# Kernel optimization log

Measured on AMD Instinct MI355X. Metric: run time of the kernel, lower is better.

Reference implementation:

```python
import jax, jax.numpy as jnp
import numpy as np

MEL = 80      # mel_dim
RED = 2       # reduction factor
D   = 256     # decoder_dim (== enc_output feature dim for dot attention)
E   = 128     # encoder_dim == prenet output dim
PRE = 256     # prenet hidden
B, T, L = 128, 500, 256


def _gru_cell(x, h, w_ih, w_hh, b_ih, b_hh):
    # PyTorch GRUCell math
    gi = x @ w_ih.T + b_ih
    gh = h @ w_hh.T + b_hh
    i_r, i_z, i_n = jnp.split(gi, 3, axis=-1)
    h_r, h_z, h_n = jnp.split(gh, 3, axis=-1)
    r = jax.nn.sigmoid(i_r + h_r)
    z = jax.nn.sigmoid(i_z + h_z)
    n = jnp.tanh(i_n + r * h_n)
    return (1.0 - z) * n + z * h


def setup_inputs() -> dict:
    key = jax.random.key(0)
    ks = jax.random.split(key, 16)
    def p(k, shape, s=0.05):
        return jax.random.normal(k, shape, dtype=jnp.float32) * s
    z = lambda n: jnp.zeros((n,), jnp.float32)
    return {
        'dec_input':  jax.random.normal(ks[0], (B, T, MEL), jnp.float32),
        'enc_output': jax.random.normal(ks[1], (B, L, D), jnp.float32),
        # prenet: mel -> 256 -> 128 (ReLU; dropout omitted for determinism)
        'pre_w1': p(ks[2], (PRE, MEL)), 'pre_b1': z(PRE),
        'pre_w2': p(ks[3], (E, PRE)),   'pre_b2': z(E),
        # attention GRUCell(encoder_dim -> decoder_dim)
        'attn_wih': p(ks[4], (3 * D, E)), 'attn_whh': p(ks[5], (3 * D, D)),
        'attn_bih': z(3 * D), 'attn_bhh': z(3 * D),
        # proj1: 2*decoder_dim -> decoder_dim
        'proj1_w': p(ks[6], (D, 2 * D)), 'proj1_b': z(D),
        # decoder GRUCells
        'rnn1_wih': p(ks[7], (3 * D, D)), 'rnn1_whh': p(ks[8], (3 * D, D)),
        'rnn1_bih': z(3 * D), 'rnn1_bhh': z(3 * D),
        'rnn2_wih': p(ks[9], (3 * D, D)), 'rnn2_whh': p(ks[10], (3 * D, D)),
        'rnn2_bih': z(3 * D), 'rnn2_bhh': z(3 * D),
        # proj2: decoder_dim -> mel_dim * reduction
        'proj2_w': p(ks[11], (MEL * RED, D)), 'proj2_b': z(MEL * RED),
    }


def reference(dec_input, enc_output,
              pre_w1, pre_b1, pre_w2, pre_b2,
              attn_wih, attn_whh, attn_bih, attn_bhh,
              proj1_w, proj1_b,
              rnn1_wih, rnn1_whh, rnn1_bih, rnn1_bhh,
              rnn2_wih, rnn2_whh, rnn2_bih, rnn2_bhh,
              proj2_w, proj2_b):
    b, t, _ = dec_input.shape

    def step(carry, frame):
        h_attn, h1, h2 = carry
        # prenet
        x = jax.nn.relu(frame @ pre_w1.T + pre_b1)
        x = jax.nn.relu(x @ pre_w2.T + pre_b2)
        # attention RNN
        h_attn = _gru_cell(x, h_attn, attn_wih, attn_whh, attn_bih, attn_bhh)
        # Luong dot attention: query = h_attn [b, D]
        scores = jnp.einsum('bd,bld->bl', h_attn, enc_output)   # [b, L]
        align = jax.nn.softmax(scores, axis=-1)
        ctx = jnp.einsum('bl,bld->bd', align, enc_output)        # [b, D]
        dec_in = jnp.concatenate([ctx, h_attn], axis=-1) @ proj1_w.T + proj1_b
        # residual GRU stack
        h1 = _gru_cell(dec_in, h1, rnn1_wih, rnn1_whh, rnn1_bih, rnn1_bhh)
        y1 = dec_in + h1
        h2 = _gru_cell(y1, h2, rnn2_wih, rnn2_whh, rnn2_bih, rnn2_bhh)
        y2 = y1 + h2
        out = y2 @ proj2_w.T + proj2_b                            # [b, MEL*RED]
        return (h_attn, h1, h2), (out, align)

    init = tuple(jnp.zeros((b, D), dec_input.dtype) for _ in range(3))
    _, (outs, aligns) = jax.lax.scan(step, init, jnp.swapaxes(dec_input, 0, 1))
    mel_out = jnp.swapaxes(outs, 0, 1).reshape(b, t * RED, MEL)  # [b, T*RED, MEL]
    alignment = jnp.transpose(aligns, (1, 2, 0))                 # [b, L, T]
    return mel_out, alignment
```

## Files before the change

### kernel.cpp

```cpp
#include <hip/hip_runtime.h>
#include <cmath>

#define B_   128
#define T_   500
#define MEL_ 80
#define RED_ 2
#define D_   256
#define E_   128
#define PRE_ 256
#define L_   256
#define TPB  1024
#define ENC_STRIDE 264
#define PTT  10

__device__ __forceinline__ float sigmoidf_(float x) { return 1.f / (1.f + expf(-x)); }
__device__ __forceinline__ float bflo(unsigned u) { return __uint_as_float(u << 16); }
__device__ __forceinline__ float bfhi(unsigned u) { return __uint_as_float(u & 0xFFFF0000u); }
__device__ __forceinline__ float bfval(ushort v) { return __uint_as_float(((unsigned)v) << 16); }
__device__ __forceinline__ ushort f2bf(float f) {
    unsigned u = __float_as_uint(f);
    return (ushort)((u + 0x7FFFu + ((u >> 16) & 1u)) >> 16);
}

__device__ __forceinline__ float acc8(uint4 u, const float* vv, float s) {
    s = fmaf(bflo(u.x), vv[0], s);
    s = fmaf(bfhi(u.x), vv[1], s);
    s = fmaf(bflo(u.y), vv[2], s);
    s = fmaf(bfhi(u.y), vv[3], s);
    s = fmaf(bflo(u.z), vv[4], s);
    s = fmaf(bfhi(u.z), vv[5], s);
    s = fmaf(bflo(u.w), vv[6], s);
    s = fmaf(bfhi(u.w), vv[7], s);
    return s;
}

template<int CH>
__device__ __forceinline__ float dotpk(const ushort* __restrict__ wp, int t, const float* v) {
    const uint4* w = reinterpret_cast<const uint4*>(wp) + (t >> 6) * (CH * 64) + (t & 63);
    float s0 = 0.f, s1 = 0.f, s2 = 0.f, s3 = 0.f;
#pragma unroll 2
    for (int c = 0; c < (CH & ~3); c += 4) {
        uint4 u0 = w[(c + 0) * 64];
        uint4 u1 = w[(c + 1) * 64];
        uint4 u2 = w[(c + 2) * 64];
        uint4 u3 = w[(c + 3) * 64];
        s0 = acc8(u0, v + (c + 0) * 8, s0);
        s1 = acc8(u1, v + (c + 1) * 8, s1);
        s2 = acc8(u2, v + (c + 2) * 8, s2);
        s3 = acc8(u3, v + (c + 3) * 8, s3);
    }
    if (CH & 2) {
        constexpr int c0 = CH & ~3;
        uint4 u0 = w[(c0 + 0) * 64];
        uint4 u1 = w[(c0 + 1) * 64];
        s0 = acc8(u0, v + (c0 + 0) * 8, s0);
        s1 = acc8(u1, v + (c0 + 1) * 8, s1);
    }
    return (s0 + s1) + (s2 + s3);
}

__device__ __forceinline__ float dotbf(const ushort* __restrict__ wrow,
                                       const float* v, int k8) {
    const uint4* w = reinterpret_cast<const uint4*>(wrow);
    float s = 0.f;
#pragma unroll 8
    for (int k = 0; k < k8; ++k) {
        uint4 u = w[k];
        const float* vv = v + k * 8;
        s = fmaf(bflo(u.x), vv[0], s);
        s = fmaf(bfhi(u.x), vv[1], s);
        s = fmaf(bflo(u.y), vv[2], s);
        s = fmaf(bfhi(u.y), vv[3], s);
        s = fmaf(bflo(u.z), vv[4], s);
        s = fmaf(bfhi(u.z), vv[5], s);
        s = fmaf(bflo(u.w), vv[6], s);
        s = fmaf(bfhi(u.w), vv[7], s);
    }
    return s;
}

__global__ void pack_bf16_kernel(const float* __restrict__ src,
                                 ushort* __restrict__ dst,
                                 int NT, int CH, int dA, int mA, int mB) {
    int i = blockIdx.x * blockDim.x + threadIdx.x;
    int n = NT * CH * 8;
    if (i >= n) return;
    int i4 = i >> 3, e = i & 7;
    int lane = i4 & 63;
    int q = i4 >> 6;
    int c = q % CH;
    int g = q / CH;
    int t = g * 64 + lane;
    dst[i] = f2bf(src[(t / dA) * mA + (t % dA) * mB + c * 8 + e]);
}

__global__ __launch_bounds__(256) void prenet_gi_kernel(
    const float* __restrict__ dec_input,
    const float* __restrict__ pre_w1, const float* __restrict__ pre_b1,
    const float* __restrict__ pre_w2, const float* __restrict__ pre_b2,
    const float* __restrict__ attn_wih, const float* __restrict__ attn_bih,
    ushort* __restrict__ gi_out)
{
    const int blk = blockIdx.x;
    const int b   = blk / (T_ / PTT);
    const int t0  = (blk % (T_ / PTT)) * PTT;
    const int tid = threadIdx.x;

    __shared__ float fr[PTT][MEL_];
    __shared__ float x1[PTT][PRE_];
    __shared__ float x2[PTT][E_];

    for (int i = tid; i < PTT * MEL_; i += 256) {
        int f = i / MEL_, m = i - f * MEL_;
        fr[f][m] = dec_input[((size_t)b * T_ + t0 + f) * MEL_ + m];
    }
    __syncthreads();

    {
        float acc[PTT];
#pragma unroll
        for (int f = 0; f < PTT; ++f) acc[f] = pre_b1[tid];
        const float4* wr = reinterpret_cast<const float4*>(pre_w1 + tid * MEL_);
        for (int k4 = 0; k4 < MEL_ / 4; ++k4) {
            float4 w = wr[k4];
#pragma unroll
            for (int f = 0; f < PTT; ++f) {
                const float* fp = &fr[f][k4 * 4];
                acc[f] = fmaf(w.x, fp[0], fmaf(w.y, fp[1], fmaf(w.z, fp[2], fmaf(w.w, fp[3], acc[f]))));
            }
        }
#pragma unroll
        for (int f = 0; f < PTT; ++f) x1[f][tid] = fmaxf(acc[f], 0.f);
    }
    __syncthreads();

    if (tid < E_) {
        float acc[PTT];
#pragma unroll
        for (int f = 0; f < PTT; ++f) acc[f] = pre_b2[tid];
        const float4* wr = reinterpret_cast<const float4*>(pre_w2 + tid * PRE_);
        for (int k4 = 0; k4 < PRE_ / 4; ++k4) {
            float4 w = wr[k4];
#pragma unroll
            for (int f = 0; f < PTT; ++f) {
                const float* fp = &x1[f][k4 * 4];
                acc[f] = fmaf(w.x, fp[0], fmaf(w.y, fp[1], fmaf(w.z, fp[2], fmaf(w.w, fp[3], acc[f]))));
            }
        }
#pragma unroll
        for (int f = 0; f < PTT; ++f) x2[f][tid] = fmaxf(acc[f], 0.f);
    }
    __syncthreads();

    for (int r = tid; r < 3 * D_; r += 256) {
        float acc[PTT];
#pragma unroll
        for (int f = 0; f < PTT; ++f) acc[f] = attn_bih[r];
        const float4* wr = reinterpret_cast<const float4*>(attn_wih + r * E_);
        for (int k4 = 0; k4 < E_ / 4; ++k4) {
            float4 w = wr[k4];
#pragma unroll
            for (int f = 0; f < PTT; ++f) {
                const float* fp = &x2[f][k4 * 4];
                acc[f] = fmaf(w.x, fp[0], fmaf(w.y, fp[1], fmaf(w.z, fp[2], fmaf(w.w, fp[3], acc[f]))));
            }
        }
#pragma unroll
        for (int f = 0; f < PTT; ++f)
            gi_out[((size_t)b * T_ + t0 + f) * (3 * D_) + r] = f2bf(acc[f]);
    }
}

__global__ __launch_bounds__(TPB, 4) void decoder_persist(
    const float* __restrict__ dec_input,
    const float* __restrict__ enc_output,
    const ushort* __restrict__ pre_w1, const float* __restrict__ pre_b1,
    const ushort* __restrict__ pre_w2, const float* __restrict__ pre_b2,
    const ushort* __restrict__ attn_wih, const ushort* __restrict__ attn_whh,
    const float* __restrict__ attn_bih, const float* __restrict__ attn_bhh,
    const ushort* __restrict__ proj1_w, const float* __restrict__ proj1_b,
    const ushort* __restrict__ rnn1_wih, const ushort* __restrict__ rnn1_whh,
    const float* __restrict__ rnn1_bih, const float* __restrict__ rnn1_bhh,
    const ushort* __restrict__ rnn2_wih, const ushort* __restrict__ rnn2_whh,
    const float* __restrict__ rnn2_bih, const float* __restrict__ rnn2_bhh,
    const ushort* __restrict__ proj2_w, const float* __restrict__ proj2_b,
    const ushort* __restrict__ gi_g,
    float* __restrict__ mel_out,
    float* __restrict__ align_out)
{
    const int b    = blockIdx.x;
    const int tid  = threadIdx.x;
    const int lane = tid & 63;
    const int wv   = tid >> 6;

    __shared__ __align__(16) ushort s_enc[L_ * ENC_STRIDE];
    __shared__ __align__(16) float A[1536];
    __shared__ __align__(16) float Bp[1536];
    __shared__ __align__(16) float s_frame[MEL_];
    __shared__ __align__(16) float s_x1[PRE_];
    __shared__ __align__(16) float s_x[E_];
    __shared__ __align__(16) float s_ha[D_];
    __shared__ __align__(16) float s_h1[D_];
    __shared__ __align__(16) float s_h2[D_];
    __shared__ __align__(16) float s_dec[D_];
    __shared__ __align__(16) float s_y1[D_];
    __shared__ __align__(16) float s_y2[D_];
    __shared__ __align__(16) float s_cat[2 * D_];
    __shared__ __align__(16) float s_al[L_];
    __shared__ float s_pmax[4];
    __shared__ float s_psum[4];

    {
        const float4* eb = reinterpret_cast<const float4*>(enc_output + (size_t)b * L_ * D_);
        for (int i = tid; i < (L_ * D_) / 4; i += TPB) {
            float4 f = eb[i];
            int row = i >> 6;
            int c4  = i & 63;
            uint2 pk;
            pk.x = (unsigned)f2bf(f.x) | ((unsigned)f2bf(f.y) << 16);
            pk.y = (unsigned)f2bf(f.z) | ((unsigned)f2bf(f.w) << 16);
            *reinterpret_cast<uint2*>(s_enc + row * ENC_STRIDE + c4 * 4) = pk;
        }
    }
    if (tid < D_) { s_ha[tid] = 0.f; s_h1[tid] = 0.f; s_h2[tid] = 0.f; }
    __syncthreads();

    auto gru_gates = [&](const ushort* wihP, const ushort* whhP,
                         const float* xin, const float* h) {
        for (int task = tid; task < 3072; task += TPB) {
            if (task < 1536) {
                A[task] = dotpk<16>(wihP, task, xin + (task & 1) * 128);
            } else {
                int u = task - 1536;
                Bp[u] = dotpk<16>(whhP, u, h + (u & 1) * 128);
            }
        }
    };
    auto gru_combine = [&](const float* bih, const float* bhh,
                           float* h, const float* xin, float* y) {
        if (tid < D_) {
            int t0 = tid;
            float gir = A[2 * t0] + A[2 * t0 + 1] + bih[t0];
            float giz = A[2 * (D_ + t0)] + A[2 * (D_ + t0) + 1] + bih[D_ + t0];
            float gin = A[2 * (2 * D_ + t0)] + A[2 * (2 * D_ + t0) + 1] + bih[2 * D_ + t0];
            float ghr = Bp[2 * t0] + Bp[2 * t0 + 1] + bhh[t0];
            float ghz = Bp[2 * (D_ + t0)] + Bp[2 * (D_ + t0) + 1] + bhh[D_ + t0];
            float ghn = Bp[2 * (2 * D_ + t0)] + Bp[2 * (2 * D_ + t0) + 1] + bhh[2 * D_ + t0];
            float r = sigmoidf_(gir + ghr);
            float z = sigmoidf_(giz + ghz);
            float n = tanhf(gin + r * ghn);
            float hn = (1.f - z) * n + z * h[t0];
            h[t0] = hn;
            y[t0] = xin[t0] + hn;
        }
    };

    for (int t = 0; t < T_; ++t) {
        if (gi_g) {
            for (int task = tid; task < 1536; task += TPB)
                Bp[task] = dotpk<16>(attn_whh, task, s_ha + (task & 1) * 128);
            __syncthreads();
        } else {
            if (tid < MEL_)
                s_frame[tid] = dec_input[((size_t)b * T_ + t) * MEL_ + tid];
            __syncthreads();
            if (tid < PRE_)
                s_x1[tid] = fmaxf(dotpk<10>(pre_w1, tid, s_frame) + pre_b1[tid], 0.f);
            __syncthreads();
            {
                int p = tid >> 7, j = tid & 127;
                A[p * 128 + j] = dotpk<4>(pre_w2, tid, s_x1 + p * 32);
            }
            __syncthreads();
            if (tid < E_) {
                float s = pre_b2[tid];
#pragma unroll
                for (int p = 0; p < 8; ++p) s += A[p * 128 + tid];
                s_x[tid] = fmaxf(s, 0.f);
            }
            __syncthreads();
            for (int task = tid; task < 2304; task += TPB) {
                if (task < 1536) {
                    Bp[task] = dotpk<16>(attn_whh, task, s_ha + (task & 1) * 128);
                } else {
                    int r2 = task - 1536;
                    A[r2] = dotpk<16>(attn_wih, r2, s_x);
                }
            }
            __syncthreads();
        }

        if (tid < D_) {
            float gir, giz, gin;
            if (gi_g) {
                const ushort* gp = gi_g + ((size_t)b * T_ + t) * (3 * D_);
                gir = bfval(gp[tid]);
                giz = bfval(gp[D_ + tid]);
                gin = bfval(gp[2 * D_ + tid]);
            } else {
                gir = A[tid] + attn_bih[tid];
                giz = A[D_ + tid] + attn_bih[D_ + tid];
                gin = A[2 * D_ + tid] + attn_bih[2 * D_ + tid];
            }
            float ghr = Bp[2 * tid] + Bp[2 * tid + 1] + attn_bhh[tid];
            float ghz = Bp[2 * (D_ + tid)] + Bp[2 * (D_ + tid) + 1] + attn_bhh[D_ + tid];
            float ghn = Bp[2 * (2 * D_ + tid)] + Bp[2 * (2 * D_ + tid) + 1] + attn_bhh[2 * D_ + tid];
            float r = sigmoidf_(gir + ghr);
            float z = sigmoidf_(giz + ghz);
            float n = tanhf(gin + r * ghn);
            s_ha[tid] = (1.f - z) * n + z * s_ha[tid];
        }
        __syncthreads();

        {
            int p = tid >> 8, l = tid & 255;
            A[p * 256 + l] = dotbf(s_enc + l * ENC_STRIDE + p * 64, s_ha + p * 64, 8);
        }
        __syncthreads();
        float sc = 0.f, e = 0.f;
        if (tid < L_) {
            sc = A[tid] + A[256 + tid] + A[512 + tid] + A[768 + tid];
            float m = sc;
            for (int o = 32; o > 0; o >>= 1) m = fmaxf(m, __shfl_xor(m, o, 64));
            if (lane == 0) s_pmax[wv] = m;
        }
        __syncthreads();
        if (tid < L_) {
            float mm = fmaxf(fmaxf(s_pmax[0], s_pmax[1]), fmaxf(s_pmax[2], s_pmax[3]));
            e = expf(sc - mm);
            float sm = e;
            for (int o = 32; o > 0; o >>= 1) sm += __shfl_xor(sm, o, 64);
            if (lane == 0) s_psum[wv] = sm;
        }
        __syncthreads();
        if (tid < L_) {
            float denom = s_psum[0] + s_psum[1] + s_psum[2] + s_psum[3];
            float al = e / denom;
            s_al[tid] = al;
            align_out[((size_t)b * L_ + tid) * T_ + t] = al;
        }
        __syncthreads();

        {
            int p = tid >> 8, d = tid & 255;
            const ushort* base = s_enc + (p * 64) * ENC_STRIDE + d;
            const float* alp = s_al + p * 64;
            float c = 0.f;
#pragma unroll 8
            for (int l = 0; l < 64; ++l)
                c = fmaf(alp[l], bfval(base[l * ENC_STRIDE]), c);
            A[p * 256 + d] = c;
        }
        __syncthreads();
        if (tid < D_) {
            float c = A[tid] + A[256 + tid] + A[512 + tid] + A[768 + tid];
            s_cat[tid]      = c;
            s_cat[D_ + tid] = s_ha[tid];
        }
        __syncthreads();

        {
            int p = tid >> 8;
            A[tid] = dotpk<16>(proj1_w, tid, s_cat + p * 128);
        }
        __syncthreads();
        if (tid < D_)
            s_dec[tid] = A[tid] + A[256 + tid] + A[512 + tid] + A[768 + tid] + proj1_b[tid];
        __syncthreads();

        gru_gates(rnn1_wih, rnn1_whh, s_dec, s_h1);
        __syncthreads();
        gru_combine(rnn1_bih, rnn1_bhh, s_h1, s_dec, s_y1);
        __syncthreads();

        gru_gates(rnn2_wih, rnn2_whh, s_y1, s_h2);
        __syncthreads();
        gru_combine(rnn2_bih, rnn2_bhh, s_h2, s_y1, s_y2);
        __syncthreads();

        if (tid < 640) {
            A[tid] = dotpk<8>(proj2_w, tid, s_y2 + (tid & 3) * 64);
        }
        __syncthreads();
        if (tid < MEL_ * RED_) {
            float s = A[4 * tid] + A[4 * tid + 1] + A[4 * tid + 2] + A[4 * tid + 3] + proj2_b[tid];
            mel_out[(size_t)b * (T_ * RED_ * MEL_) + (size_t)t * (MEL_ * RED_) + tid] = s;
        }
    }
}

extern "C" void kernel_launch(void* const* d_in, const int* in_sizes, int n_in,
                              void* d_out, int out_size, void* d_ws, size_t ws_size,
                              hipStream_t stream) {
    const float* dec_input = (const float*)d_in[0];
    const float* enc_output= (const float*)d_in[1];
    const float* pre_w1    = (const float*)d_in[2];
    const float* pre_b1    = (const float*)d_in[3];
    const float* pre_w2    = (const float*)d_in[4];
    const float* pre_b2    = (const float*)d_in[5];
    const float* attn_wih  = (const float*)d_in[6];
    const float* attn_whh  = (const float*)d_in[7];
    const float* attn_bih  = (const float*)d_in[8];
    const float* attn_bhh  = (const float*)d_in[9];
    const float* proj1_w   = (const float*)d_in[10];
    const float* proj1_b   = (const float*)d_in[11];
    const float* rnn1_wih  = (const float*)d_in[12];
    const float* rnn1_whh  = (const float*)d_in[13];
    const float* rnn1_bih  = (const float*)d_in[14];
    const float* rnn1_bhh  = (const float*)d_in[15];
    const float* rnn2_wih  = (const float*)d_in[16];
    const float* rnn2_whh  = (const float*)d_in[17];
    const float* rnn2_bih  = (const float*)d_in[18];
    const float* rnn2_bhh  = (const float*)d_in[19];
    const float* proj2_w   = (const float*)d_in[20];
    const float* proj2_b   = (const float*)d_in[21];

    float* mel   = (float*)d_out;
    float* align = (float*)d_out + (size_t)B_ * T_ * RED_ * MEL_;

    const int n_pre_w1   = PRE_ * MEL_;
    const int n_pre_w2   = E_ * PRE_;
    const int n_attn_wih = 3 * D_ * E_;
    const int n_attn_whh = 3 * D_ * D_;
    const int n_proj1    = D_ * 2 * D_;
    const int n_rnn_w    = 3 * D_ * D_;
    const int n_proj2    = MEL_ * RED_ * D_;

    ushort* w = (ushort*)d_ws;
    ushort* c_pre_w1   = w; w += n_pre_w1;
    ushort* c_pre_w2   = w; w += n_pre_w2;
    ushort* c_attn_wih = w; w += n_attn_wih;
    ushort* c_attn_whh = w; w += n_attn_whh;
    ushort* c_proj1    = w; w += n_proj1;
    ushort* c_rnn1_wih = w; w += n_rnn_w;
    ushort* c_rnn1_whh = w; w += n_rnn_w;
    ushort* c_rnn2_wih = w; w += n_rnn_w;
    ushort* c_rnn2_whh = w; w += n_rnn_w;
    ushort* c_proj2    = w; w += n_proj2;

    const size_t n_gi = (size_t)B_ * T_ * 3 * D_;
    const size_t packed_bytes = (size_t)(w - (ushort*)d_ws) * sizeof(ushort);
    const size_t need = packed_bytes + n_gi * sizeof(ushort);
    ushort* c_gi = (ws_size >= need) ? w : nullptr;

    auto pack = [&](const float* src, ushort* dst, int NT, int CH, int dA, int mA, int mB) {
        int n = NT * CH * 8;
        pack_bf16_kernel<<<dim3((n + 255) / 256), dim3(256), 0, stream>>>(
            src, dst, NT, CH, dA, mA, mB);
    };
    pack(pre_w1,   c_pre_w1,   256,  10, 1,   80,  0);
    pack(pre_w2,   c_pre_w2,   1024, 4,  128, 32,  256);
    pack(attn_wih, c_attn_wih, 768,  16, 1,   128, 0);
    pack(attn_whh, c_attn_whh, 1536, 16, 2,   256, 128);
    pack(proj1_w,  c_proj1,    1024, 16, 256, 128, 512);
    pack(rnn1_wih, c_rnn1_wih, 1536, 16, 2,   256, 128);
    pack(rnn1_whh, c_rnn1_whh, 1536, 16, 2,   256, 128);
    pack(rnn2_wih, c_rnn2_wih, 1536, 16, 2,   256, 128);
    pack(rnn2_whh, c_rnn2_whh, 1536, 16, 2,   256, 128);
    pack(proj2_w,  c_proj2,    640,  8,  4,   256, 64);

    if (c_gi) {
        prenet_gi_kernel<<<dim3(B_ * (T_ / PTT)), dim3(256), 0, stream>>>(
            dec_input, pre_w1, pre_b1, pre_w2, pre_b2, attn_wih, attn_bih, c_gi);
    }

    decoder_persist<<<dim3(B_), dim3(TPB), 0, stream>>>(
        dec_input, enc_output,
        c_pre_w1, pre_b1, c_pre_w2, pre_b2,
        c_attn_wih, c_attn_whh, attn_bih, attn_bhh,
        c_proj1, proj1_b,
        c_rnn1_wih, c_rnn1_whh, rnn1_bih, rnn1_bhh,
        c_rnn2_wih, c_rnn2_whh, rnn2_bih, rnn2_bhh,
        c_proj2, proj2_b,
        c_gi,
        mel, align);
}
```

Baseline: 15.45 ms.

## Batch recurrent matvecs, swizzle encoder smem, and chunk precomputed input gates

The three hidden-state matvecs (attention, rnn1 and rnn2 W_hh) are now computed together in one pass at the start of each step, which removes two barrier-separated phases per step. The encoder tile in shared memory drops its padded stride in favour of an XOR swizzle, to avoid bank conflicts while using less LDS. The fallback in-kernel prenet path is removed. Precomputed input gates are produced in batch chunks sized to the workspace, so the precompute path always runs, at the cost of possibly serializing the kernels when the workspace is small.

```diff
diff --git a/kernel.cpp b/kernel.cpp
--- a/kernel.cpp
+++ b/kernel.cpp
@@ -10,7 +10,7 @@
 #define PRE_ 256
 #define L_   256
 #define TPB  1024
-#define ENC_STRIDE 264
+#define ENC_C 256
 #define PTT  10
 
 __device__ __forceinline__ float sigmoidf_(float x) { return 1.f / (1.f + expf(-x)); }
@@ -59,26 +59,6 @@
     return (s0 + s1) + (s2 + s3);
 }
 
-__device__ __forceinline__ float dotbf(const ushort* __restrict__ wrow,
-                                       const float* v, int k8) {
-    const uint4* w = reinterpret_cast<const uint4*>(wrow);
-    float s = 0.f;
-#pragma unroll 8
-    for (int k = 0; k < k8; ++k) {
-        uint4 u = w[k];
-        const float* vv = v + k * 8;
-        s = fmaf(bflo(u.x), vv[0], s);
-        s = fmaf(bfhi(u.x), vv[1], s);
-        s = fmaf(bflo(u.y), vv[2], s);
-        s = fmaf(bfhi(u.y), vv[3], s);
-        s = fmaf(bflo(u.z), vv[4], s);
-        s = fmaf(bfhi(u.z), vv[5], s);
-        s = fmaf(bflo(u.w), vv[6], s);
-        s = fmaf(bfhi(u.w), vv[7], s);
-    }
-    return s;
-}
-
 __global__ void pack_bf16_kernel(const float* __restrict__ src,
                                  ushort* __restrict__ dst,
                                  int NT, int CH, int dA, int mA, int mB) {
@@ -99,10 +79,12 @@
     const float* __restrict__ pre_w1, const float* __restrict__ pre_b1,
     const float* __restrict__ pre_w2, const float* __restrict__ pre_b2,
     const float* __restrict__ attn_wih, const float* __restrict__ attn_bih,
-    ushort* __restrict__ gi_out)
+    ushort* __restrict__ gi_out,
+    int b0)
 {
     const int blk = blockIdx.x;
-    const int b   = blk / (T_ / PTT);
+    const int bl  = blk / (T_ / PTT);
+    const int b   = b0 + bl;
     const int t0  = (blk % (T_ / PTT)) * PTT;
     const int tid = threadIdx.x;
 
@@ -167,17 +149,13 @@
         }
 #pragma unroll
         for (int f = 0; f < PTT; ++f)
-            gi_out[((size_t)b * T_ + t0 + f) * (3 * D_) + r] = f2bf(acc[f]);
+            gi_out[((size_t)bl * T_ + t0 + f) * (3 * D_) + r] = f2bf(acc[f]);
     }
 }
 
 __global__ __launch_bounds__(TPB, 4) void decoder_persist(
-    const float* __restrict__ dec_input,
     const float* __restrict__ enc_output,
-    const ushort* __restrict__ pre_w1, const float* __restrict__ pre_b1,
-    const ushort* __restrict__ pre_w2, const float* __restrict__ pre_b2,
-    const ushort* __restrict__ attn_wih, const ushort* __restrict__ attn_whh,
-    const float* __restrict__ attn_bih, const float* __restrict__ attn_bhh,
+    const ushort* __restrict__ attn_whh, const float* __restrict__ attn_bhh,
     const ushort* __restrict__ proj1_w, const float* __restrict__ proj1_b,
     const ushort* __restrict__ rnn1_wih, const ushort* __restrict__ rnn1_whh,
     const float* __restrict__ rnn1_bih, const float* __restrict__ rnn1_bhh,
@@ -185,27 +163,25 @@
     const float* __restrict__ rnn2_bih, const float* __restrict__ rnn2_bhh,
     const ushort* __restrict__ proj2_w, const float* __restrict__ proj2_b,
     const ushort* __restrict__ gi_g,
+    int b0,
     float* __restrict__ mel_out,
     float* __restrict__ align_out)
 {
-    const int b    = blockIdx.x;
+    const int b    = blockIdx.x + b0;
     const int tid  = threadIdx.x;
     const int lane = tid & 63;
     const int wv   = tid >> 6;
 
-    __shared__ __align__(16) ushort s_enc[L_ * ENC_STRIDE];
-    __shared__ __align__(16) float A[1536];
-    __shared__ __align__(16) float Bp[1536];
-    __shared__ __align__(16) float s_frame[MEL_];
-    __shared__ __align__(16) float s_x1[PRE_];
-    __shared__ __align__(16) float s_x[E_];
+    __shared__ __align__(16) ushort s_enc[L_ * ENC_C];
+    __shared__ __align__(16) float P[4608];
+    __shared__ __align__(16) float P2b[640];
     __shared__ __align__(16) float s_ha[D_];
     __shared__ __align__(16) float s_h1[D_];
     __shared__ __align__(16) float s_h2[D_];
     __shared__ __align__(16) float s_dec[D_];
     __shared__ __align__(16) float s_y1[D_];
     __shared__ __align__(16) float s_y2[D_];
-    __shared__ __align__(16) float s_cat[2 * D_];
+    __shared__ __align__(16) float s_ctx[D_];
     __shared__ __align__(16) float s_al[L_];
     __shared__ float s_pmax[4];
     __shared__ float s_psum[4];
@@ -216,36 +192,29 @@
             float4 f = eb[i];
             int row = i >> 6;
             int c4  = i & 63;
+            int c    = c4 >> 1;
+            int half = c4 & 1;
+            int slot = (c & 24) | ((c & 7) ^ (row & 7));
             uint2 pk;
             pk.x = (unsigned)f2bf(f.x) | ((unsigned)f2bf(f.y) << 16);
             pk.y = (unsigned)f2bf(f.z) | ((unsigned)f2bf(f.w) << 16);
-            *reinterpret_cast<uint2*>(s_enc + row * ENC_STRIDE + c4 * 4) = pk;
+            *reinterpret_cast<uint2*>(s_enc + row * ENC_C + slot * 8 + half * 4) = pk;
         }
     }
     if (tid < D_) { s_ha[tid] = 0.f; s_h1[tid] = 0.f; s_h2[tid] = 0.f; }
     __syncthreads();
 
-    auto gru_gates = [&](const ushort* wihP, const ushort* whhP,
-                         const float* xin, const float* h) {
-        for (int task = tid; task < 3072; task += TPB) {
-            if (task < 1536) {
-                A[task] = dotpk<16>(wihP, task, xin + (task & 1) * 128);
-            } else {
-                int u = task - 1536;
-                Bp[u] = dotpk<16>(whhP, u, h + (u & 1) * 128);
-            }
-        }
-    };
-    auto gru_combine = [&](const float* bih, const float* bhh,
+    auto gru_combine = [&](const float* gip, const float* ghp,
+                           const float* bih, const float* bhh,
                            float* h, const float* xin, float* y) {
         if (tid < D_) {
             int t0 = tid;
-            float gir = A[2 * t0] + A[2 * t0 + 1] + bih[t0];
-            float giz = A[2 * (D_ + t0)] + A[2 * (D_ + t0) + 1] + bih[D_ + t0];
-            float gin = A[2 * (2 * D_ + t0)] + A[2 * (2 * D_ + t0) + 1] + bih[2 * D_ + t0];
-            float ghr = Bp[2 * t0] + Bp[2 * t0 + 1] + bhh[t0];
-            float ghz = Bp[2 * (D_ + t0)] + Bp[2 * (D_ + t0) + 1] + bhh[D_ + t0];
-            float ghn = Bp[2 * (2 * D_ + t0)] + Bp[2 * (2 * D_ + t0) + 1] + bhh[2 * D_ + t0];
+            float gir = gip[2 * t0] + gip[2 * t0 + 1] + bih[t0];
+            float giz = gip[2 * (D_ + t0)] + gip[2 * (D_ + t0) + 1] + bih[D_ + t0];
+            float gin = gip[2 * (2 * D_ + t0)] + gip[2 * (2 * D_ + t0) + 1] + bih[2 * D_ + t0];
+            float ghr = ghp[2 * t0] + ghp[2 * t0 + 1] + bhh[t0];
+            float ghz = ghp[2 * (D_ + t0)] + ghp[2 * (D_ + t0) + 1] + bhh[D_ + t0];
+            float ghn = ghp[2 * (2 * D_ + t0)] + ghp[2 * (2 * D_ + t0) + 1] + bhh[2 * D_ + t0];
             float r = sigmoidf_(gir + ghr);
             float z = sigmoidf_(giz + ghz);
             float n = tanhf(gin + r * ghn);
@@ -256,55 +225,23 @@
     };
 
     for (int t = 0; t < T_; ++t) {
-        if (gi_g) {
-            for (int task = tid; task < 1536; task += TPB)
-                Bp[task] = dotpk<16>(attn_whh, task, s_ha + (task & 1) * 128);
-            __syncthreads();
-        } else {
-            if (tid < MEL_)
-                s_frame[tid] = dec_input[((size_t)b * T_ + t) * MEL_ + tid];
-            __syncthreads();
-            if (tid < PRE_)
-                s_x1[tid] = fmaxf(dotpk<10>(pre_w1, tid, s_frame) + pre_b1[tid], 0.f);
-            __syncthreads();
-            {
-                int p = tid >> 7, j = tid & 127;
-                A[p * 128 + j] = dotpk<4>(pre_w2, tid, s_x1 + p * 32);
-            }
-            __syncthreads();
-            if (tid < E_) {
-                float s = pre_b2[tid];
-#pragma unroll
-                for (int p = 0; p < 8; ++p) s += A[p * 128 + tid];
-                s_x[tid] = fmaxf(s, 0.f);
-            }
-            __syncthreads();
-            for (int task = tid; task < 2304; task += TPB) {
-                if (task < 1536) {
-                    Bp[task] = dotpk<16>(attn_whh, task, s_ha + (task & 1) * 128);
-                } else {
-                    int r2 = task - 1536;
-                    A[r2] = dotpk<16>(attn_wih, r2, s_x);
-                }
-            }
-            __syncthreads();
-        }
+        for (int task = tid; task < 4608; task += TPB) {
+            const ushort* wP; const float* hv; int u;
+            if (task < 1536)      { wP = attn_whh; hv = s_ha; u = task; }
+            else if (task < 3072) { wP = rnn1_whh; hv = s_h1; u = task - 1536; }
+            else                  { wP = rnn2_whh; hv = s_h2; u = task - 3072; }
+            P[task] = dotpk<16>(wP, u, hv + (u & 1) * 128);
+        }
+        __syncthreads();
 
         if (tid < D_) {
-            float gir, giz, gin;
-            if (gi_g) {
-                const ushort* gp = gi_g + ((size_t)b * T_ + t) * (3 * D_);
-                gir = bfval(gp[tid]);
-                giz = bfval(gp[D_ + tid]);
-                gin = bfval(gp[2 * D_ + tid]);
-            } else {
-                gir = A[tid] + attn_bih[tid];
-                giz = A[D_ + tid] + attn_bih[D_ + tid];
-                gin = A[2 * D_ + tid] + attn_bih[2 * D_ + tid];
-            }
-            float ghr = Bp[2 * tid] + Bp[2 * tid + 1] + attn_bhh[tid];
-            float ghz = Bp[2 * (D_ + tid)] + Bp[2 * (D_ + tid) + 1] + attn_bhh[D_ + tid];
-            float ghn = Bp[2 * (2 * D_ + tid)] + Bp[2 * (2 * D_ + tid) + 1] + attn_bhh[2 * D_ + tid];
+            const ushort* gp = gi_g + ((size_t)blockIdx.x * T_ + t) * (3 * D_);
+            float gir = bfval(gp[tid]);
+            float giz = bfval(gp[D_ + tid]);
+            float gin = bfval(gp[2 * D_ + tid]);
+            float ghr = P[2 * tid] + P[2 * tid + 1] + attn_bhh[tid];
+            float ghz = P[2 * (D_ + tid)] + P[2 * (D_ + tid) + 1] + attn_bhh[D_ + tid];
+            float ghn = P[2 * (2 * D_ + tid)] + P[2 * (2 * D_ + tid) + 1] + attn_bhh[2 * D_ + tid];
             float r = sigmoidf_(gir + ghr);
             float z = sigmoidf_(giz + ghz);
             float n = tanhf(gin + r * ghn);
@@ -314,12 +251,27 @@
 
         {
             int p = tid >> 8, l = tid & 255;
-            A[p * 256 + l] = dotbf(s_enc + l * ENC_STRIDE + p * 64, s_ha + p * 64, 8);
+            const uint4* rowp = reinterpret_cast<const uint4*>(s_enc + l * ENC_C) + p * 8;
+            const float* v = s_ha + p * 64;
+            int rot = l & 7;
+            float a0 = 0.f, a1 = 0.f, a2 = 0.f, a3 = 0.f;
+#pragma unroll
+            for (int k = 0; k < 8; k += 4) {
+                uint4 u0 = rowp[(k + 0) ^ rot];
+                uint4 u1 = rowp[(k + 1) ^ rot];
+                uint4 u2 = rowp[(k + 2) ^ rot];
+                uint4 u3 = rowp[(k + 3) ^ rot];
+                a0 = acc8(u0, v + (k + 0) * 8, a0);
+                a1 = acc8(u1, v + (k + 1) * 8, a1);
+                a2 = acc8(u2, v + (k + 2) * 8, a2);
+                a3 = acc8(u3, v + (k + 3) * 8, a3);
+            }
+            P[p * 256 + l] = (a0 + a1) + (a2 + a3);
         }
         __syncthreads();
         float sc = 0.f, e = 0.f;
         if (tid < L_) {
-            sc = A[tid] + A[256 + tid] + A[512 + tid] + A[768 + tid];
+            sc = P[tid] + P[256 + tid] + P[512 + tid] + P[768 + tid];
             float m = sc;
             for (int o = 32; o > 0; o >>= 1) m = fmaxf(m, __shfl_xor(m, o, 64));
             if (lane == 0) s_pmax[wv] = m;
@@ -343,47 +295,54 @@
 
         {
             int p = tid >> 8, d = tid & 255;
-            const ushort* base = s_enc + (p * 64) * ENC_STRIDE + d;
+            int chigh = (d >> 3) & 24, clow = (d >> 3) & 7, el = d & 7;
             const float* alp = s_al + p * 64;
-            float c = 0.f;
-#pragma unroll 8
-            for (int l = 0; l < 64; ++l)
-                c = fmaf(alp[l], bfval(base[l * ENC_STRIDE]), c);
-            A[p * 256 + d] = c;
-        }
-        __syncthreads();
-        if (tid < D_) {
-            float c = A[tid] + A[256 + tid] + A[512 + tid] + A[768 + tid];
-            s_cat[tid]      = c;
-            s_cat[D_ + tid] = s_ha[tid];
-        }
+            float a0 = 0.f, a1 = 0.f;
+            for (int l8 = 0; l8 < 8; ++l8) {
+                const ushort* rb = s_enc + (p * 64 + l8 * 8) * ENC_C;
+                const float* al8 = alp + l8 * 8;
+#pragma unroll
+                for (int dr = 0; dr < 8; ++dr) {
+                    int slot = chigh | (clow ^ dr);
+                    float vv = bfval(rb[dr * ENC_C + slot * 8 + el]);
+                    if (dr & 1) a1 = fmaf(al8[dr], vv, a1);
+                    else        a0 = fmaf(al8[dr], vv, a0);
+                }
+            }
+            P[p * 256 + d] = a0 + a1;
+        }
+        __syncthreads();
+        if (tid < D_)
+            s_ctx[tid] = P[tid] + P[256 + tid] + P[512 + tid] + P[768 + tid];
         __syncthreads();
 
         {
             int p = tid >> 8;
-            A[tid] = dotpk<16>(proj1_w, tid, s_cat + p * 128);
+            const float* v = (p < 2) ? (s_ctx + p * 128) : (s_ha + (p - 2) * 128);
+            P[tid] = dotpk<16>(proj1_w, tid, v);
         }
         __syncthreads();
         if (tid < D_)
-            s_dec[tid] = A[tid] + A[256 + tid] + A[512 + tid] + A[768 + tid] + proj1_b[tid];
-        __syncthreads();
-
-        gru_gates(rnn1_wih, rnn1_whh, s_dec, s_h1);
-        __syncthreads();
-        gru_combine(rnn1_bih, rnn1_bhh, s_h1, s_dec, s_y1);
-        __syncthreads();
-
-        gru_gates(rnn2_wih, rnn2_whh, s_y1, s_h2);
-        __syncthreads();
-        gru_combine(rnn2_bih, rnn2_bhh, s_h2, s_y1, s_y2);
-        __syncthreads();
-
-        if (tid < 640) {
-            A[tid] = dotpk<8>(proj2_w, tid, s_y2 + (tid & 3) * 64);
-        }
+            s_dec[tid] = P[tid] + P[256 + tid] + P[512 + tid] + P[768 + tid] + proj1_b[tid];
+        __syncthreads();
+
+        for (int task = tid; task < 1536; task += TPB)
+            P[task] = dotpk<16>(rnn1_wih, task, s_dec + (task & 1) * 128);
+        __syncthreads();
+        gru_combine(P, P + 1536, rnn1_bih, rnn1_bhh, s_h1, s_dec, s_y1);
+        __syncthreads();
+
+        for (int task = tid; task < 1536; task += TPB)
+            P[task] = dotpk<16>(rnn2_wih, task, s_y1 + (task & 1) * 128);
+        __syncthreads();
+        gru_combine(P, P + 3072, rnn2_bih, rnn2_bhh, s_h2, s_y1, s_y2);
+        __syncthreads();
+
+        if (tid < 640)
+            P2b[tid] = dotpk<8>(proj2_w, tid, s_y2 + (tid & 3) * 64);
         __syncthreads();
         if (tid < MEL_ * RED_) {
-            float s = A[4 * tid] + A[4 * tid + 1] + A[4 * tid + 2] + A[4 * tid + 3] + proj2_b[tid];
+            float s = P2b[4 * tid] + P2b[4 * tid + 1] + P2b[4 * tid + 2] + P2b[4 * tid + 3] + proj2_b[tid];
             mel_out[(size_t)b * (T_ * RED_ * MEL_) + (size_t)t * (MEL_ * RED_) + tid] = s;
         }
     }
@@ -418,39 +377,25 @@
     float* mel   = (float*)d_out;
     float* align = (float*)d_out + (size_t)B_ * T_ * RED_ * MEL_;
 
-    const int n_pre_w1   = PRE_ * MEL_;
-    const int n_pre_w2   = E_ * PRE_;
-    const int n_attn_wih = 3 * D_ * E_;
-    const int n_attn_whh = 3 * D_ * D_;
-    const int n_proj1    = D_ * 2 * D_;
-    const int n_rnn_w    = 3 * D_ * D_;
-    const int n_proj2    = MEL_ * RED_ * D_;
+    const int n_whh   = 3 * D_ * D_;
+    const int n_proj1 = D_ * 2 * D_;
+    const int n_proj2 = MEL_ * RED_ * D_;
 
     ushort* w = (ushort*)d_ws;
-    ushort* c_pre_w1   = w; w += n_pre_w1;
-    ushort* c_pre_w2   = w; w += n_pre_w2;
-    ushort* c_attn_wih = w; w += n_attn_wih;
-    ushort* c_attn_whh = w; w += n_attn_whh;
+    ushort* c_attn_whh = w; w += n_whh;
     ushort* c_proj1    = w; w += n_proj1;
-    ushort* c_rnn1_wih = w; w += n_rnn_w;
-    ushort* c_rnn1_whh = w; w += n_rnn_w;
-    ushort* c_rnn2_wih = w; w += n_rnn_w;
-    ushort* c_rnn2_whh = w; w += n_rnn_w;
+    ushort* c_rnn1_wih = w; w += n_whh;
+    ushort* c_rnn1_whh = w; w += n_whh;
+    ushort* c_rnn2_wih = w; w += n_whh;
+    ushort* c_rnn2_whh = w; w += n_whh;
     ushort* c_proj2    = w; w += n_proj2;
-
-    const size_t n_gi = (size_t)B_ * T_ * 3 * D_;
-    const size_t packed_bytes = (size_t)(w - (ushort*)d_ws) * sizeof(ushort);
-    const size_t need = packed_bytes + n_gi * sizeof(ushort);
-    ushort* c_gi = (ws_size >= need) ? w : nullptr;
+    ushort* c_gi       = w;
 
     auto pack = [&](const float* src, ushort* dst, int NT, int CH, int dA, int mA, int mB) {
         int n = NT * CH * 8;
         pack_bf16_kernel<<<dim3((n + 255) / 256), dim3(256), 0, stream>>>(
             src, dst, NT, CH, dA, mA, mB);
     };
-    pack(pre_w1,   c_pre_w1,   256,  10, 1,   80,  0);
-    pack(pre_w2,   c_pre_w2,   1024, 4,  128, 32,  256);
-    pack(attn_wih, c_attn_wih, 768,  16, 1,   128, 0);
     pack(attn_whh, c_attn_whh, 1536, 16, 2,   256, 128);
     pack(proj1_w,  c_proj1,    1024, 16, 256, 128, 512);
     pack(rnn1_wih, c_rnn1_wih, 1536, 16, 2,   256, 128);
@@ -459,19 +404,26 @@
     pack(rnn2_whh, c_rnn2_whh, 1536, 16, 2,   256, 128);
     pack(proj2_w,  c_proj2,    640,  8,  4,   256, 64);
 
-    if (c_gi) {
-        prenet_gi_kernel<<<dim3(B_ * (T_ / PTT)), dim3(256), 0, stream>>>(
-            dec_input, pre_w1, pre_b1, pre_w2, pre_b2, attn_wih, attn_bih, c_gi);
-    }
-
-    decoder_persist<<<dim3(B_), dim3(TPB), 0, stream>>>(
-        dec_input, enc_output,
-        c_pre_w1, pre_b1, c_pre_w2, pre_b2,
-        c_attn_wih, c_attn_whh, attn_bih, attn_bhh,
-        c_proj1, proj1_b,
-        c_rnn1_wih, c_rnn1_whh, rnn1_bih, rnn1_bhh,
-        c_rnn2_wih, c_rnn2_whh, rnn2_bih, rnn2_bhh,
-        c_proj2, proj2_b,
-        c_gi,
-        mel, align);
-}
+    const size_t packed_elems = (size_t)(w - (ushort*)d_ws);
+    const size_t gi_per_b = (size_t)T_ * 3 * D_;
+    size_t avail = (ws_size / 2 > packed_elems) ? (ws_size / 2 - packed_elems) : 0;
+    int bchunk = (int)(avail / gi_per_b);
+    if (bchunk > B_) bchunk = B_;
+    if (bchunk < 1)  bchunk = 1;
+
+    for (int b0 = 0; b0 < B_; b0 += bchunk) {
+        int nb = (b0 + bchunk <= B_) ? bchunk : (B_ - b0);
+        prenet_gi_kernel<<<dim3(nb * (T_ / PTT)), dim3(256), 0, stream>>>(
+            dec_input, pre_w1, pre_b1, pre_w2, pre_b2, attn_wih, attn_bih,
+            c_gi, b0);
+        decoder_persist<<<dim3(nb), dim3(TPB), 0, stream>>>(
+            enc_output,
+            c_attn_whh, attn_bhh,
+            c_proj1, proj1_b,
+            c_rnn1_wih, c_rnn1_whh, rnn1_bih, rnn1_bhh,
+            c_rnn2_wih, c_rnn2_whh, rnn2_bih, rnn2_bhh,
+            c_proj2, proj2_b,
+            c_gi, b0,
+            mel, align);
+    }
+}
```

Measured after the change: 15.53 ms. Within noise of the previous version (+0.5%).
